# Optimization experiments

Hardware: AMD Instinct MI355X
Metric: run time of the kernel (lower is better)

The kernel has to match this reference:

```python
import jax, jax.numpy as jnp
import numpy as np

B, L, C = 4, 1024, 512
H, DK, DV, NF = 8, 64, 192, 192


def _sinusoid_basis(seq_len, nf):
    # distances -(L-1)..(L-1), sinusoidal feature basis of width nf
    d = jnp.arange(-(seq_len - 1), seq_len, dtype=jnp.float32)[:, None]  # [2L-1,1]
    half = nf // 2
    freqs = jnp.exp(-jnp.arange(half, dtype=jnp.float32) * (np.log(10000.0) / half))
    ang = d * freqs[None, :]
    return jnp.concatenate([jnp.sin(ang), jnp.cos(ang)], axis=-1)  # [2L-1, nf]


def setup_inputs() -> dict:
    key = jax.random.key(0)
    ks = jax.random.split(key, 12)
    s = lambda fan: 1.0 / np.sqrt(fan)
    return {
        "x": jax.random.normal(ks[0], (B, L, C), jnp.float32),
        "Wq": jax.random.normal(ks[1], (C, H * DK), jnp.float32) * s(C),
        "bq": jnp.zeros((H * DK,), jnp.float32),
        "Wk": jax.random.normal(ks[2], (C, H * DK), jnp.float32) * s(C),
        "bk": jnp.zeros((H * DK,), jnp.float32),
        "Wv": jax.random.normal(ks[3], (C, H * DV), jnp.float32) * s(C),
        "bv": jnp.zeros((H * DV,), jnp.float32),
        "Wo": jax.random.normal(ks[4], (H * DV, C), jnp.float32) * s(H * DV),
        "bo": jnp.zeros((C,), jnp.float32),
        "We": jax.random.normal(ks[5], (NF, DK), jnp.float32) * s(NF),
        "u": jax.random.normal(ks[6], (H, DK), jnp.float32) * 0.02,
        "v": jax.random.normal(ks[7], (H, DK), jnp.float32) * 0.02,
    }


def reference(x, Wq, bq, Wk, bk, Wv, bv, Wo, bo, We, u, v):
    b, l, c = x.shape
    Q = (x @ Wq + bq).reshape(b, l, H, DK).transpose(0, 2, 1, 3)  # [b,h,l,dk]
    K = (x @ Wk + bk).reshape(b, l, H, DK).transpose(0, 2, 1, 3)
    V = (x @ Wv + bv).reshape(b, l, H, DV).transpose(0, 2, 1, 3)  # [b,h,l,dv]

    R = _sinusoid_basis(l, NF) @ We  # [2l-1, dk], index r <-> distance r-(l-1)

    # rel-shift gather: shifted[i,j] = raw[i, j - i + (l-1)] (relative distance j-i)
    idx = (jnp.arange(l)[None, :] - jnp.arange(l)[:, None]) + (l - 1)  # [l,l]

    term1 = jnp.einsum('bhid,bhjd->bhij', Q, K)                 # content-content
    t2 = jnp.einsum('bhid,rd->bhir', Q, R)                      # [b,h,l,2l-1]
    term2 = jnp.take_along_axis(t2, jnp.broadcast_to(idx[None, None], (b, H, l, l)), axis=-1)
    term3 = jnp.einsum('hd,bhjd->bhj', u, K)[:, :, None, :]     # content bias [b,h,1,l]
    t4 = jnp.einsum('hd,rd->hr', v, R)                          # [h,2l-1]
    term4 = jnp.take(t4, idx, axis=1)[None]                     # [1,h,l,l]

    attn = jax.nn.softmax(term1 + term2 + term3 + term4, axis=-1)
    out = jnp.einsum('bhij,bhjd->bhid', attn, V)                # [b,h,l,dv]
    out = out.transpose(0, 2, 1, 3).reshape(b, l, H * DV)
    return out @ Wo + bo
```

## Files before the change

### kernel.cpp

```cpp
#include <hip/hip_runtime.h>
#include <cstdint>
#include <cstddef>

#define B_   4
#define L_   1024
#define H_   8
#define DK_  64
#define DV_  192
#define HALF_ 96
#define LOG2E_ 1.44269504088896f

typedef _Float16 half8 __attribute__((ext_vector_type(8)));
typedef _Float16 half4v __attribute__((ext_vector_type(4)));
typedef float f32x4 __attribute__((ext_vector_type(4)));

__device__ __forceinline__ void gll16(const void* g, void* lds) {
    __builtin_amdgcn_global_load_lds(
        (const __attribute__((address_space(1))) unsigned int*)g,
        (__attribute__((address_space(3))) unsigned int*)lds, 16, 0, 0);
}

__global__ void k_prologue(const float* __restrict__ x, _Float16* __restrict__ xh,
                           const float* __restrict__ We, _Float16* __restrict__ Weh,
                           const float* __restrict__ Wq, const float* __restrict__ Wk,
                           const float* __restrict__ Wv, const float* __restrict__ Wo,
                           _Float16* __restrict__ Wqkvt, _Float16* __restrict__ Wot,
                           const float* __restrict__ bq, const float* __restrict__ bk,
                           const float* __restrict__ bv, float* __restrict__ bqkv,
                           float* __restrict__ Tsin, float* __restrict__ Tcos,
                           const float* __restrict__ v, float* __restrict__ vWe) {
    __shared__ float tile[64][65];
    const int t = blockIdx.x, tid = threadIdx.x;
    if (t < 2048) {
        int i = t * 256 + tid;
        float4 vv = ((const float4*)x)[i];
        half4v h;
        h[0] = (_Float16)vv.x; h[1] = (_Float16)vv.y; h[2] = (_Float16)vv.z; h[3] = (_Float16)vv.w;
        ((half4v*)xh)[i] = h;
    } else if (t < 2060) {
        int i = (t - 2048) * 256 + tid;
        if (i < 192 * 64 / 4) {
            float4 vv = ((const float4*)We)[i];
            half4v h;
            h[0] = (_Float16)vv.x; h[1] = (_Float16)vv.y; h[2] = (_Float16)vv.z; h[3] = (_Float16)vv.w;
            ((half4v*)Weh)[i] = h;
        }
    } else if (t < 2572) {
        const float* src; _Float16* dst; int K, N, bx, by;
        if (t < 2124)      { int rel = t - 2060; src = Wq; dst = Wqkvt;                       K = 512;  N = 512;  bx = rel & 7;   by = rel >> 3; }
        else if (t < 2188) { int rel = t - 2124; src = Wk; dst = Wqkvt + (size_t)512 * 512;   K = 512;  N = 512;  bx = rel & 7;   by = rel >> 3; }
        else if (t < 2380) { int rel = t - 2188; src = Wv; dst = Wqkvt + (size_t)1024 * 512;  K = 512;  N = 1536; bx = rel % 24;  by = rel / 24; }
        else               { int rel = t - 2380; src = Wo; dst = Wot;                         K = 1536; N = 512;  bx = rel & 7;   by = rel >> 3; }
        int n0 = bx << 6, k0 = by << 6;
#pragma unroll
        for (int q = 0; q < 16; ++q) {
            int e = (q << 8) + tid;
            int r = e >> 6, c = e & 63;
            tile[r][c] = src[(size_t)(k0 + r) * N + n0 + c];
        }
        __syncthreads();
#pragma unroll
        for (int q = 0; q < 16; ++q) {
            int e = (q << 8) + tid;
            int r = e >> 6, c = e & 63;
            dst[(size_t)(n0 + r) * K + k0 + c] = (_Float16)tile[c][r];
        }
    } else if (t < 2582) {
        int i = (t - 2572) * 256 + tid;
        if (i < 2560) {
            float vv;
            if (i < 512) vv = bq[i];
            else if (i < 1024) vv = bk[i - 512];
            else vv = bv[i - 1024];
            bqkv[i] = vv;
        }
    } else if (t < 2966) {
        int idx = (t - 2582) * 256 + tid;
        if (idx < L_ * HALF_) {
            int i = idx / HALF_;
            int f = idx - i * HALF_;
            float w = expf(-(float)f * 0.09594104554141865f);
            float a = (float)i * w;
            Tsin[idx] = sinf(a);
            Tcos[idx] = cosf(a);
        }
    } else {
        int idx = (t - 2966) * 256 + tid;
        if (idx < 8 * 192) {
            int h = idx / 192, f = idx - h * 192;
            float acc = 0.f;
#pragma unroll
            for (int k4 = 0; k4 < 16; ++k4) {
                float4 vv = *(const float4*)(v + (h << 6) + (k4 << 2));
                float4 we = *(const float4*)(We + (size_t)f * 64 + (k4 << 2));
                acc += vv.x * we.x + vv.y * we.y + vv.z * we.z + vv.w * we.w;
            }
            vWe[idx] = acc;
        }
    }
}

template<int TNB, bool OUT_F16, bool GMODE>
__global__ __launch_bounds__(256) void k_gemm2(
    const _Float16* __restrict__ A, const _Float16* __restrict__ Bt,
    const float* __restrict__ bias, void* __restrict__ Cout,
    int M, int N, int K, int nbx)
{
    constexpr int BUFSZ = 16384 + TNB * 128;
    __shared__ char sm[2 * BUFSZ];
    const int nwg = gridDim.x;
    const int bid = blockIdx.x;
    const int sw = (bid & 7) * (nwg >> 3) + (bid >> 3);
    const int bx = sw % nbx, by = sw / nbx;
    const int m0 = by << 7, n0 = bx * TNB;
    const int tid = threadIdx.x;
    const int lane = tid & 63, l15 = lane & 15, g = lane >> 4;
    const int w = tid >> 6;
    constexpr int AM = (TNB == 128) ? 4 : 2;
    constexpr int BJ = (TNB >= 64) ? 4 : 2;
    const int wm = (TNB == 128) ? ((w >> 1) << 6) : (w << 5);
    const int wn = (TNB == 128) ? ((w & 1) << 6) : 0;

    f32x4 acc[AM][BJ] = {};

    auto stage = [&](int kt, int bufsel) {
        char* As = sm + bufsel * BUFSZ;
        char* Bs = As + 16384;
#pragma unroll
        for (int i2 = 0; i2 < 4; ++i2) {
            int byte = (i2 << 12) + (tid << 4);
            int row = byte >> 7, bso = byte & 127;
            size_t a_off;
            if constexpr (GMODE) {
                int rg = m0 + row;
                a_off = ((((size_t)(rg >> 13) << 10) + (rg & 1023)) * 2560 + (((rg >> 10) & 7) << 6) + (kt << 6)) * 2;
            } else {
                a_off = ((size_t)(m0 + row) * K + (kt << 6)) * 2;
            }
            gll16((const char*)A + a_off + (bso ^ ((row & 7) << 4)), As + byte);
        }
        const char* Bg = (const char*)Bt + ((size_t)n0 * K + (kt << 6)) * 2;
#pragma unroll
        for (int i2 = 0; i2 < (TNB >> 5); ++i2) {
            int byte = (i2 << 12) + (tid << 4);
            int row = byte >> 7, bso = byte & 127;
            gll16(Bg + (size_t)row * (K * 2) + (bso ^ ((row & 7) << 4)), Bs + byte);
        }
    };

    const int nk = K >> 6;
    stage(0, 0);
    __syncthreads();
    for (int kt = 0; kt < nk; ++kt) {
        const int cur = kt & 1;
        if (kt + 1 < nk) stage(kt + 1, cur ^ 1);
        const char* As = sm + cur * BUFSZ;
        const char* Bs = As + 16384;
#pragma unroll
        for (int kq = 0; kq < 2; ++kq) {
            half8 af[AM], bf[BJ];
#pragma unroll
            for (int a = 0; a < AM; ++a) {
                int row = wm + (a << 4) + l15;
                af[a] = *(const half8*)(As + (row << 7) + ((((kq << 2) | g) ^ (row & 7)) << 4));
            }
#pragma unroll
            for (int bj = 0; bj < BJ; ++bj) {
                int row = wn + (bj << 4) + l15;
                bf[bj] = *(const half8*)(Bs + (row << 7) + ((((kq << 2) | g) ^ (row & 7)) << 4));
            }
#pragma unroll
            for (int a = 0; a < AM; ++a)
#pragma unroll
                for (int bj = 0; bj < BJ; ++bj)
                    acc[a][bj] = __builtin_amdgcn_mfma_f32_16x16x32_f16(af[a], bf[bj], acc[a][bj], 0, 0, 0);
        }
        __syncthreads();
    }
#pragma unroll
    for (int a = 0; a < AM; ++a)
#pragma unroll
        for (int bj = 0; bj < BJ; ++bj)
#pragma unroll
            for (int r = 0; r < 4; ++r) {
                int row = m0 + wm + (a << 4) + (g << 2) + r;
                int col = n0 + wn + (bj << 4) + l15;
                float bb;
                if constexpr (GMODE) bb = bias[(((m0 >> 10) & 7) * N) + col];
                else                 bb = bias ? bias[col] : 0.0f;
                float vv = acc[a][bj][r] + bb;
                if (OUT_F16) ((_Float16*)Cout)[(size_t)row * N + col] = (_Float16)vv;
                else         ((float*)Cout)[(size_t)row * N + col] = vv;
            }
}

__global__ void k_build(const _Float16* __restrict__ QKVh, const _Float16* __restrict__ Gf,
                        const float* __restrict__ Tsin, const float* __restrict__ Tcos,
                        const float* __restrict__ u,
                        _Float16* __restrict__ Qext, _Float16* __restrict__ Kext,
                        float* __restrict__ bias3, _Float16* __restrict__ Vd) {
    __shared__ float tile[64][65];
    const int t = blockIdx.x, tid = threadIdx.x;
    if (t < 8192) {
        const bool isQ = (t < 4096);
        int r = ((isQ ? t : t - 4096) << 3) + (tid >> 5);
        int cc = tid & 31;
        int i = r & 1023, h = (r >> 10) & 7, b = r >> 13;
        half8 val;
        if (cc < 8) {
            if (isQ) {
                half8 q = *(const half8*)(QKVh + ((size_t)(b << 10) + i) * 2560 + (h << 6) + (cc << 3));
#pragma unroll
                for (int z = 0; z < 8; ++z) val[z] = (_Float16)((float)q[z] * LOG2E_);
            } else {
                val = *(const half8*)(QKVh + ((size_t)(b << 10) + i) * 2560 + 512 + (h << 6) + (cc << 3));
                float4 u0 = *(const float4*)(u + (h << 6) + (cc << 3));
                float4 u1 = *(const float4*)(u + (h << 6) + (cc << 3) + 4);
                float p = (float)val[0] * u0.x + (float)val[1] * u0.y + (float)val[2] * u0.z + (float)val[3] * u0.w
                        + (float)val[4] * u1.x + (float)val[5] * u1.y + (float)val[6] * u1.z + (float)val[7] * u1.w;
                p += __shfl_xor(p, 1); p += __shfl_xor(p, 2); p += __shfl_xor(p, 4);
                if (cc == 0) bias3[r] = p * LOG2E_;
            }
        } else {
            int f = (cc < 20) ? ((cc - 8) << 3) : ((cc - 20) << 3);
            if (isQ) {
                half8 g0 = *(const half8*)(Gf + (size_t)r * 192 + f);
                half8 g1 = *(const half8*)(Gf + (size_t)r * 192 + 96 + f);
                float4 s0 = *(const float4*)(Tsin + i * 96 + f);
                float4 s1 = *(const float4*)(Tsin + i * 96 + f + 4);
                float4 c0 = *(const float4*)(Tcos + i * 96 + f);
                float4 c1 = *(const float4*)(Tcos + i * 96 + f + 4);
                float sv[8] = {s0.x, s0.y, s0.z, s0.w, s1.x, s1.y, s1.z, s1.w};
                float cv[8] = {c0.x, c0.y, c0.z, c0.w, c1.x, c1.y, c1.z, c1.w};
                if (cc < 20) {
#pragma unroll
                    for (int z = 0; z < 8; ++z) val[z] = (_Float16)(((float)g0[z] * cv[z] + (float)g1[z] * sv[z]) * LOG2E_);
                } else {
#pragma unroll
                    for (int z = 0; z < 8; ++z) val[z] = (_Float16)(((float)g1[z] * cv[z] - (float)g0[z] * sv[z]) * LOG2E_);
                }
            } else {
                const float* T = (cc < 20) ? Tsin : Tcos;
                float4 t0 = *(const float4*)(T + i * 96 + f);
                float4 t1 = *(const float4*)(T + i * 96 + f + 4);
                float tv[8] = {t0.x, t0.y, t0.z, t0.w, t1.x, t1.y, t1.z, t1.w};
#pragma unroll
                for (int z = 0; z < 8; ++z) val[z] = (_Float16)tv[z];
            }
        }
        _Float16* dst = isQ ? Qext : Kext;
        *(half8*)((char*)dst + (size_t)r * 512 + ((cc ^ (r & 7)) << 4)) = val;
    } else {
        int rel = t - 8192;
        int jx = rel & 15, rest = rel >> 4;
        int dy = rest % 3, bh = rest / 3;
        int j0 = jx << 6, d0 = dy << 6;
        int b = bh >> 3, h = bh & 7;
#pragma unroll
        for (int q = 0; q < 16; ++q) {
            int e = (q << 8) + tid;
            int r = e >> 6, c = e & 63;
            tile[r][c] = (float)QKVh[((size_t)(b << 10) + j0 + r) * 2560 + 1024 + h * 192 + d0 + c];
        }
        __syncthreads();
        char* outb = (char*)Vd + (size_t)bh * 192 * 2048;
#pragma unroll
        for (int q = 0; q < 2; ++q) {
            int e = (q << 8) + tid;
            int dr = e >> 3, jc = e & 7;
            int d = d0 + dr;
            half8 v;
#pragma unroll
            for (int z = 0; z < 8; ++z) v[z] = (_Float16)tile[(jc << 3) + z][dr];
            *(half8*)(outb + (size_t)d * 2048 + (j0 << 1) + ((jc ^ (d & 7)) << 4)) = v;
        }
    }
}

__global__ __attribute__((amdgpu_flat_work_group_size(1024, 1024)))
void k_attn(
    const _Float16* __restrict__ Qext, const _Float16* __restrict__ Kext,
    const _Float16* __restrict__ Vd, const float* __restrict__ bias3,
    _Float16* __restrict__ AOh)
{
    __shared__ char smem[131072];

    const int bid = blockIdx.x;
    const int sw = ((bid & 7) << 5) + (bid >> 3);
    const int bh = sw >> 3;
    const int i0 = (sw & 7) << 7;
    const int tid = threadIdx.x;
    const int w = tid >> 6, lane = tid & 63, l15 = lane & 15, g = lane >> 4;
    const int rowg = w & 7, jhalf = w >> 3;
    const int b = bh >> 3, h = bh & 7;

    const char* Kg = (const char*)Kext + ((size_t)bh << 10) * 512;
    const char* Vg = (const char*)Vd + (size_t)bh * 192 * 2048;
    const float* b3g = bias3 + (bh << 10);
    char* Pw = smem + 114688 + (w << 10);

    half8 qf[8];
    {
        int row = i0 + (rowg << 4) + l15;
        const char* qp = (const char*)Qext + ((size_t)(bh << 10) + row) * 512;
#pragma unroll
        for (int kq = 0; kq < 8; ++kq)
            qf[kq] = *(const half8*)(qp + ((((kq << 2) + g) ^ (row & 7)) << 4));
    }

    f32x4 oacc[12] = {};
    float m_run[4], l_lane[4];
#pragma unroll
    for (int r = 0; r < 4; ++r) { m_run[r] = -3.0e38f; l_lane[r] = 0.f; }

    auto stage = [&](int jt, int bufsel) {
        char* Kb = smem + bufsel * 32768;
        char* Vb = smem + 65536 + bufsel * 24576;
        const char* Ksrc = Kg + (size_t)jt * 32768;
#pragma unroll
        for (int i2 = 0; i2 < 2; ++i2) {
            int byte = (i2 << 14) + (tid << 4);
            gll16(Ksrc + byte, Kb + byte);
        }
        {
            int byte = tid << 4;
            int d = byte >> 7, c = byte & 127;
            gll16(Vg + (size_t)d * 2048 + (jt << 7) + c, Vb + byte);
        }
        if (tid < 512) {
            int byte = 16384 + (tid << 4);
            int d = byte >> 7, c = byte & 127;
            gll16(Vg + (size_t)d * 2048 + (jt << 7) + c, Vb + byte);
        }
    };

    stage(0, 0);
    __syncthreads();

    for (int jt = 0; jt < 16; ++jt) {
        const int cur = jt & 1;
        if (jt + 1 < 16) stage(jt + 1, cur ^ 1);
        const char* Kb = smem + cur * 32768;
        const char* Vb = smem + 65536 + cur * 24576;

        f32x4 s[2];
#pragma unroll
        for (int jn = 0; jn < 2; ++jn) {
            float b3 = b3g[(jt << 6) + (jhalf << 5) + (jn << 4) + l15];
            s[jn] = (f32x4){b3, b3, b3, b3};
        }
        __builtin_amdgcn_s_setprio(1);
#pragma unroll
        for (int kq = 0; kq < 8; ++kq) {
#pragma unroll
            for (int jn = 0; jn < 2; ++jn) {
                int krow = (((jhalf << 1) + jn) << 4) + l15;
                half8 bf = *(const half8*)(Kb + (krow << 9) + ((((kq << 2) + g) ^ (krow & 7)) << 4));
                s[jn] = __builtin_amdgcn_mfma_f32_16x16x32_f16(qf[kq], bf, s[jn], 0, 0, 0);
            }
        }
        __builtin_amdgcn_s_setprio(0);
        bool pass = true;
#pragma unroll
        for (int jn = 0; jn < 2; ++jn)
#pragma unroll
            for (int r = 0; r < 4; ++r) pass &= (s[jn][r] <= m_run[r] + 8.0f);
        if (!__all(pass)) {
#pragma unroll
            for (int r = 0; r < 4; ++r) {
                float tm = fmaxf(s[0][r], s[1][r]);
                tm = fmaxf(tm, __shfl_xor(tm, 1));
                tm = fmaxf(tm, __shfl_xor(tm, 2));
                tm = fmaxf(tm, __shfl_xor(tm, 4));
                tm = fmaxf(tm, __shfl_xor(tm, 8));
                float mnew = fmaxf(m_run[r], tm);
                float al = exp2f(m_run[r] - mnew);
                l_lane[r] *= al;
                m_run[r] = mnew;
#pragma unroll
                for (int dn = 0; dn < 12; ++dn) oacc[dn][r] *= al;
            }
        }
#pragma unroll
        for (int jn = 0; jn < 2; ++jn)
#pragma unroll
            for (int r = 0; r < 4; ++r) {
                float p = exp2f(s[jn][r] - m_run[r]);
                l_lane[r] += p;
                int row = (g << 2) + r;
                int c = ((jn << 1) + (l15 >> 3)) ^ g;
                *(_Float16*)(Pw + (row << 6) + (c << 4) + ((l15 & 7) << 1)) = (_Float16)p;
            }
        half8 pa;
        {
            int c = g ^ ((l15 >> 2) & 3);
            pa = *(const half8*)(Pw + (l15 << 6) + (c << 4));
        }
        __builtin_amdgcn_s_setprio(1);
#pragma unroll
        for (int dn = 0; dn < 12; ++dn) {
            int d = (dn << 4) + l15;
            half8 vb = *(const half8*)(Vb + (d << 7) + ((((jhalf << 2) + g) ^ (d & 7)) << 4));
            oacc[dn] = __builtin_amdgcn_mfma_f32_16x16x32_f16(pa, vb, oacc[dn], 0, 0, 0);
        }
        __builtin_amdgcn_s_setprio(0);
        __syncthreads();
    }

    float l_run[4];
#pragma unroll
    for (int r = 0; r < 4; ++r) {
        float l = l_lane[r];
        l += __shfl_xor(l, 1);
        l += __shfl_xor(l, 2);
        l += __shfl_xor(l, 4);
        l += __shfl_xor(l, 8);
        l_run[r] = l;
    }

    float* Cml = (float*)smem;
    float* Co  = (float*)(smem + 2048);
#pragma unroll
    for (int r = 0; r < 4; ++r)
        if (l15 == 0) {
            int rowi = (rowg << 4) + (g << 2) + r;
            Cml[(((jhalf << 7) + rowi) << 1) + 0] = m_run[r];
            Cml[(((jhalf << 7) + rowi) << 1) + 1] = l_run[r];
        }
    __syncthreads();
    float fs[4], lt[4];
#pragma unroll
    for (int r = 0; r < 4; ++r) {
        int rowi = (rowg << 4) + (g << 2) + r;
        float mo = Cml[((((1 - jhalf) << 7) + rowi) << 1) + 0];
        float lo = Cml[((((1 - jhalf) << 7) + rowi) << 1) + 1];
        float M = fmaxf(m_run[r], mo);
        float f0 = exp2f(m_run[r] - M);
        float f1 = exp2f(mo - M);
        fs[r] = f0;
        lt[r] = l_run[r] * f0 + lo * f1;
    }
    if (jhalf == 1) {
#pragma unroll
        for (int dn = 0; dn < 12; ++dn)
#pragma unroll
            for (int r = 0; r < 4; ++r) {
                int rowi = (rowg << 4) + (g << 2) + r;
                Co[rowi * 196 + (dn << 4) + l15] = oacc[dn][r] * fs[r];
            }
    }
    __syncthreads();
    if (jhalf == 0) {
#pragma unroll
        for (int r = 0; r < 4; ++r) {
            int rowi = (rowg << 4) + (g << 2) + r;
            float inv = 1.0f / lt[r];
#pragma unroll
            for (int dn = 0; dn < 12; ++dn) {
                float ov = (oacc[dn][r] * fs[r] + Co[rowi * 196 + (dn << 4) + l15]) * inv;
                AOh[((size_t)(b << 10) + i0 + rowi) * 1536 + h * 192 + (dn << 4) + l15] = (_Float16)ov;
            }
        }
    }
}

extern "C" void kernel_launch(void* const* d_in, const int* in_sizes, int n_in,
                              void* d_out, int out_size, void* d_ws, size_t ws_size,
                              hipStream_t stream) {
    const float* x  = (const float*)d_in[0];
    const float* Wq = (const float*)d_in[1];
    const float* bq = (const float*)d_in[2];
    const float* Wk = (const float*)d_in[3];
    const float* bk = (const float*)d_in[4];
    const float* Wv = (const float*)d_in[5];
    const float* bv = (const float*)d_in[6];
    const float* Wo = (const float*)d_in[7];
    const float* bo = (const float*)d_in[8];
    const float* We = (const float*)d_in[9];
    const float* u  = (const float*)d_in[10];
    const float* v  = (const float*)d_in[11];
    float* out = (float*)d_out;

    char* ws = (char*)d_ws;
    size_t off = 0;
    auto alloc = [&](size_t bytes) -> void* {
        void* p = ws + off;
        off += (bytes + 255) & ~(size_t)255;
        return p;
    };
    _Float16* xh    = (_Float16*)alloc((size_t)4096 * 512 * 2);
    _Float16* Weh   = (_Float16*)alloc((size_t)192 * 64 * 2);
    _Float16* Wqkvt = (_Float16*)alloc((size_t)2560 * 512 * 2);
    _Float16* Wot   = (_Float16*)alloc((size_t)512 * 1536 * 2);
    float*    bqkv  = (float*)alloc((size_t)2560 * 4);
    float*    Tsin  = (float*)alloc((size_t)1024 * 96 * 4);
    float*    Tcos  = (float*)alloc((size_t)1024 * 96 * 4);
    float*    vWe   = (float*)alloc((size_t)8 * 192 * 4);
    _Float16* QKVh  = (_Float16*)alloc((size_t)4096 * 2560 * 2);
    _Float16* Gf16  = (_Float16*)alloc((size_t)32768 * 192 * 2);
    _Float16* Qext  = (_Float16*)alloc((size_t)32768 * 256 * 2);
    _Float16* Kext  = (_Float16*)alloc((size_t)32768 * 256 * 2);
    float*    bias3 = (float*)alloc((size_t)32768 * 4);
    _Float16* Vd    = (_Float16*)alloc((size_t)32 * 192 * 1024 * 2);
    _Float16* AOh   = (_Float16*)alloc((size_t)4096 * 1536 * 2);
    if (off > ws_size) return;

    k_prologue<<<2972, 256, 0, stream>>>(x, xh, We, Weh, Wq, Wk, Wv, Wo,
                                         Wqkvt, Wot, bq, bk, bv, bqkv, Tsin, Tcos, v, vWe);

    k_gemm2<128, true, false><<<640, 256, 0, stream>>>(xh, Wqkvt, bqkv, QKVh, 4096, 2560, 512, 20);

    k_gemm2<64, true, true><<<768, 256, 0, stream>>>(QKVh, Weh, vWe, Gf16, 32768, 192, 64, 3);

    k_build<<<9728, 256, 0, stream>>>(QKVh, Gf16, Tsin, Tcos, u, Qext, Kext, bias3, Vd);

    k_attn<<<256, 1024, 0, stream>>>(Qext, Kext, Vd, bias3, AOh);

    k_gemm2<32, false, false><<<512, 256, 0, stream>>>(AOh, Wot, bo, out, 4096, 512, 1536, 16);
}
```

Measured before the change: 147.4 us.

## Share one trig table across heads instead of replicating extended K

```diff
diff --git a/kernel.cpp b/kernel.cpp
--- a/kernel.cpp
+++ b/kernel.cpp
@@ -28,7 +28,8 @@
                            const float* __restrict__ bq, const float* __restrict__ bk,
                            const float* __restrict__ bv, float* __restrict__ bqkv,
                            float* __restrict__ Tsin, float* __restrict__ Tcos,
-                           const float* __restrict__ v, float* __restrict__ vWe) {
+                           const float* __restrict__ v, float* __restrict__ vWe,
+                           _Float16* __restrict__ Ctrig) {
     __shared__ float tile[64][65];
     const int t = blockIdx.x, tid = threadIdx.x;
     if (t < 2048) {
@@ -84,7 +85,7 @@
             Tsin[idx] = sinf(a);
             Tcos[idx] = cosf(a);
         }
-    } else {
+    } else if (t < 2972) {
         int idx = (t - 2966) * 256 + tid;
         if (idx < 8 * 192) {
             int h = idx / 192, f = idx - h * 192;
@@ -96,6 +97,21 @@
                 acc += vv.x * we.x + vv.y * we.y + vv.z * we.z + vv.w * we.w;
             }
             vWe[idx] = acc;
+        }
+    } else {
+        int idx = (t - 2972) * 256 + tid;
+        if (idx < 1024 * 24) {
+            int j = idx / 24, lc = idx - j * 24;
+            int f0 = (lc < 12) ? (lc << 3) : ((lc - 12) << 3);
+            half8 val;
+#pragma unroll
+            for (int z = 0; z < 8; ++z) {
+                float w = expf(-(float)(f0 + z) * 0.09594104554141865f);
+                float a = (float)j * w;
+                val[z] = (_Float16)((lc < 12) ? sinf(a) : cosf(a));
+            }
+            int pos = ((lc >> 3) << 3) + ((lc & 7) ^ (j & 7));
+            *(half8*)((char*)Ctrig + (size_t)j * 384 + (pos << 4)) = val;
         }
     }
 }
@@ -197,61 +213,52 @@
 __global__ void k_build(const _Float16* __restrict__ QKVh, const _Float16* __restrict__ Gf,
                         const float* __restrict__ Tsin, const float* __restrict__ Tcos,
                         const float* __restrict__ u,
-                        _Float16* __restrict__ Qext, _Float16* __restrict__ Kext,
+                        _Float16* __restrict__ Qext, _Float16* __restrict__ Ksmall,
                         float* __restrict__ bias3, _Float16* __restrict__ Vd) {
     __shared__ float tile[64][65];
     const int t = blockIdx.x, tid = threadIdx.x;
-    if (t < 8192) {
-        const bool isQ = (t < 4096);
-        int r = ((isQ ? t : t - 4096) << 3) + (tid >> 5);
+    if (t < 4096) {
+        int r = (t << 3) + (tid >> 5);
         int cc = tid & 31;
         int i = r & 1023, h = (r >> 10) & 7, b = r >> 13;
         half8 val;
         if (cc < 8) {
-            if (isQ) {
-                half8 q = *(const half8*)(QKVh + ((size_t)(b << 10) + i) * 2560 + (h << 6) + (cc << 3));
-#pragma unroll
-                for (int z = 0; z < 8; ++z) val[z] = (_Float16)((float)q[z] * LOG2E_);
-            } else {
-                val = *(const half8*)(QKVh + ((size_t)(b << 10) + i) * 2560 + 512 + (h << 6) + (cc << 3));
-                float4 u0 = *(const float4*)(u + (h << 6) + (cc << 3));
-                float4 u1 = *(const float4*)(u + (h << 6) + (cc << 3) + 4);
-                float p = (float)val[0] * u0.x + (float)val[1] * u0.y + (float)val[2] * u0.z + (float)val[3] * u0.w
-                        + (float)val[4] * u1.x + (float)val[5] * u1.y + (float)val[6] * u1.z + (float)val[7] * u1.w;
-                p += __shfl_xor(p, 1); p += __shfl_xor(p, 2); p += __shfl_xor(p, 4);
-                if (cc == 0) bias3[r] = p * LOG2E_;
-            }
+            half8 q = *(const half8*)(QKVh + ((size_t)(b << 10) + i) * 2560 + (h << 6) + (cc << 3));
+#pragma unroll
+            for (int z = 0; z < 8; ++z) val[z] = (_Float16)((float)q[z] * LOG2E_);
         } else {
             int f = (cc < 20) ? ((cc - 8) << 3) : ((cc - 20) << 3);
-            if (isQ) {
-                half8 g0 = *(const half8*)(Gf + (size_t)r * 192 + f);
-                half8 g1 = *(const half8*)(Gf + (size_t)r * 192 + 96 + f);
-                float4 s0 = *(const float4*)(Tsin + i * 96 + f);
-                float4 s1 = *(const float4*)(Tsin + i * 96 + f + 4);
-                float4 c0 = *(const float4*)(Tcos + i * 96 + f);
-                float4 c1 = *(const float4*)(Tcos + i * 96 + f + 4);
-                float sv[8] = {s0.x, s0.y, s0.z, s0.w, s1.x, s1.y, s1.z, s1.w};
-                float cv[8] = {c0.x, c0.y, c0.z, c0.w, c1.x, c1.y, c1.z, c1.w};
-                if (cc < 20) {
-#pragma unroll
-                    for (int z = 0; z < 8; ++z) val[z] = (_Float16)(((float)g0[z] * cv[z] + (float)g1[z] * sv[z]) * LOG2E_);
-                } else {
-#pragma unroll
-                    for (int z = 0; z < 8; ++z) val[z] = (_Float16)(((float)g1[z] * cv[z] - (float)g0[z] * sv[z]) * LOG2E_);
-                }
+            half8 g0 = *(const half8*)(Gf + (size_t)r * 192 + f);
+            half8 g1 = *(const half8*)(Gf + (size_t)r * 192 + 96 + f);
+            float4 s0 = *(const float4*)(Tsin + i * 96 + f);
+            float4 s1 = *(const float4*)(Tsin + i * 96 + f + 4);
+            float4 c0 = *(const float4*)(Tcos + i * 96 + f);
+            float4 c1 = *(const float4*)(Tcos + i * 96 + f + 4);
+            float sv[8] = {s0.x, s0.y, s0.z, s0.w, s1.x, s1.y, s1.z, s1.w};
+            float cv[8] = {c0.x, c0.y, c0.z, c0.w, c1.x, c1.y, c1.z, c1.w};
+            if (cc < 20) {
+#pragma unroll
+                for (int z = 0; z < 8; ++z) val[z] = (_Float16)(((float)g0[z] * cv[z] + (float)g1[z] * sv[z]) * LOG2E_);
             } else {
-                const float* T = (cc < 20) ? Tsin : Tcos;
-                float4 t0 = *(const float4*)(T + i * 96 + f);
-                float4 t1 = *(const float4*)(T + i * 96 + f + 4);
-                float tv[8] = {t0.x, t0.y, t0.z, t0.w, t1.x, t1.y, t1.z, t1.w};
-#pragma unroll
-                for (int z = 0; z < 8; ++z) val[z] = (_Float16)tv[z];
-            }
-        }
-        _Float16* dst = isQ ? Qext : Kext;
-        *(half8*)((char*)dst + (size_t)r * 512 + ((cc ^ (r & 7)) << 4)) = val;
+#pragma unroll
+                for (int z = 0; z < 8; ++z) val[z] = (_Float16)(((float)g1[z] * cv[z] - (float)g0[z] * sv[z]) * LOG2E_);
+            }
+        }
+        *(half8*)((char*)Qext + (size_t)r * 512 + ((cc ^ (r & 7)) << 4)) = val;
+    } else if (t < 5120) {
+        int r = ((t - 4096) << 5) + (tid >> 3);
+        int cc = tid & 7;
+        int i = r & 1023, h = (r >> 10) & 7, b = r >> 13;
+        half8 val = *(const half8*)(QKVh + ((size_t)(b << 10) + i) * 2560 + 512 + (h << 6) + (cc << 3));
+        float4 u0 = *(const float4*)(u + (h << 6) + (cc << 3));
+        float4 u1 = *(const float4*)(u + (h << 6) + (cc << 3) + 4);
+        float p = (float)val[0] * u0.x + (float)val[1] * u0.y + (float)val[2] * u0.z + (float)val[3] * u0.w
+                + (float)val[4] * u1.x + (float)val[5] * u1.y + (float)val[6] * u1.z + (float)val[7] * u1.w;
+        p += __shfl_xor(p, 1); p += __shfl_xor(p, 2); p += __shfl_xor(p, 4);
+        if (cc == 0) bias3[r] = p * LOG2E_;
+        *(half8*)((char*)Ksmall + (size_t)r * 128 + ((cc ^ (r & 7)) << 4)) = val;
     } else {
-        int rel = t - 8192;
+        int rel = t - 5120;
         int jx = rel & 15, rest = rel >> 4;
         int dy = rest % 3, bh = rest / 3;
         int j0 = jx << 6, d0 = dy << 6;
@@ -279,7 +286,8 @@
 
 __global__ __attribute__((amdgpu_flat_work_group_size(1024, 1024)))
 void k_attn(
-    const _Float16* __restrict__ Qext, const _Float16* __restrict__ Kext,
+    const _Float16* __restrict__ Qext, const _Float16* __restrict__ Ksmall,
+    const _Float16* __restrict__ Ctrig,
     const _Float16* __restrict__ Vd, const float* __restrict__ bias3,
     _Float16* __restrict__ AOh)
 {
@@ -294,7 +302,8 @@
     const int rowg = w & 7, jhalf = w >> 3;
     const int b = bh >> 3, h = bh & 7;
 
-    const char* Kg = (const char*)Kext + ((size_t)bh << 10) * 512;
+    const char* Ksm = (const char*)Ksmall + ((size_t)bh << 10) * 128;
+    const char* Ctg = (const char*)Ctrig;
     const char* Vg = (const char*)Vd + (size_t)bh * 192 * 2048;
     const float* b3g = bias3 + (bh << 10);
     char* Pw = smem + 114688 + (w << 10);
@@ -316,11 +325,15 @@
     auto stage = [&](int jt, int bufsel) {
         char* Kb = smem + bufsel * 32768;
         char* Vb = smem + 65536 + bufsel * 24576;
-        const char* Ksrc = Kg + (size_t)jt * 32768;
+        const int cc = tid & 31;
 #pragma unroll
         for (int i2 = 0; i2 < 2; ++i2) {
             int byte = (i2 << 14) + (tid << 4);
-            gll16(Ksrc + byte, Kb + byte);
+            int j = (jt << 6) + (byte >> 9);
+            const char* src = (cc < 8)
+                ? Ksm + (size_t)j * 128 + (cc << 4)
+                : Ctg + (size_t)j * 384 + ((cc - 8) << 4);
+            gll16(src, Kb + byte);
         }
         {
             int byte = tid << 4;
@@ -488,33 +501,34 @@
         off += (bytes + 255) & ~(size_t)255;
         return p;
     };
-    _Float16* xh    = (_Float16*)alloc((size_t)4096 * 512 * 2);
-    _Float16* Weh   = (_Float16*)alloc((size_t)192 * 64 * 2);
-    _Float16* Wqkvt = (_Float16*)alloc((size_t)2560 * 512 * 2);
-    _Float16* Wot   = (_Float16*)alloc((size_t)512 * 1536 * 2);
-    float*    bqkv  = (float*)alloc((size_t)2560 * 4);
-    float*    Tsin  = (float*)alloc((size_t)1024 * 96 * 4);
-    float*    Tcos  = (float*)alloc((size_t)1024 * 96 * 4);
-    float*    vWe   = (float*)alloc((size_t)8 * 192 * 4);
-    _Float16* QKVh  = (_Float16*)alloc((size_t)4096 * 2560 * 2);
-    _Float16* Gf16  = (_Float16*)alloc((size_t)32768 * 192 * 2);
-    _Float16* Qext  = (_Float16*)alloc((size_t)32768 * 256 * 2);
-    _Float16* Kext  = (_Float16*)alloc((size_t)32768 * 256 * 2);
-    float*    bias3 = (float*)alloc((size_t)32768 * 4);
-    _Float16* Vd    = (_Float16*)alloc((size_t)32 * 192 * 1024 * 2);
-    _Float16* AOh   = (_Float16*)alloc((size_t)4096 * 1536 * 2);
+    _Float16* xh     = (_Float16*)alloc((size_t)4096 * 512 * 2);
+    _Float16* Weh    = (_Float16*)alloc((size_t)192 * 64 * 2);
+    _Float16* Wqkvt  = (_Float16*)alloc((size_t)2560 * 512 * 2);
+    _Float16* Wot    = (_Float16*)alloc((size_t)512 * 1536 * 2);
+    float*    bqkv   = (float*)alloc((size_t)2560 * 4);
+    float*    Tsin   = (float*)alloc((size_t)1024 * 96 * 4);
+    float*    Tcos   = (float*)alloc((size_t)1024 * 96 * 4);
+    float*    vWe    = (float*)alloc((size_t)8 * 192 * 4);
+    _Float16* Ctrig  = (_Float16*)alloc((size_t)1024 * 192 * 2);
+    _Float16* QKVh   = (_Float16*)alloc((size_t)4096 * 2560 * 2);
+    _Float16* Gf16   = (_Float16*)alloc((size_t)32768 * 192 * 2);
+    _Float16* Qext   = (_Float16*)alloc((size_t)32768 * 256 * 2);
+    _Float16* Ksmall = (_Float16*)alloc((size_t)32768 * 64 * 2);
+    float*    bias3  = (float*)alloc((size_t)32768 * 4);
+    _Float16* Vd     = (_Float16*)alloc((size_t)32 * 192 * 1024 * 2);
+    _Float16* AOh    = (_Float16*)alloc((size_t)4096 * 1536 * 2);
     if (off > ws_size) return;
 
-    k_prologue<<<2972, 256, 0, stream>>>(x, xh, We, Weh, Wq, Wk, Wv, Wo,
-                                         Wqkvt, Wot, bq, bk, bv, bqkv, Tsin, Tcos, v, vWe);
+    k_prologue<<<3068, 256, 0, stream>>>(x, xh, We, Weh, Wq, Wk, Wv, Wo,
+                                         Wqkvt, Wot, bq, bk, bv, bqkv, Tsin, Tcos, v, vWe, Ctrig);
 
     k_gemm2<128, true, false><<<640, 256, 0, stream>>>(xh, Wqkvt, bqkv, QKVh, 4096, 2560, 512, 20);
 
     k_gemm2<64, true, true><<<768, 256, 0, stream>>>(QKVh, Weh, vWe, Gf16, 32768, 192, 64, 3);
 
-    k_build<<<9728, 256, 0, stream>>>(QKVh, Gf16, Tsin, Tcos, u, Qext, Kext, bias3, Vd);
-
-    k_attn<<<256, 1024, 0, stream>>>(Qext, Kext, Vd, bias3, AOh);
+    k_build<<<6656, 256, 0, stream>>>(QKVh, Gf16, Tsin, Tcos, u, Qext, Ksmall, bias3, Vd);
+
+    k_attn<<<256, 1024, 0, stream>>>(Qext, Ksmall, Ctrig, Vd, bias3, AOh);
 
     k_gemm2<32, false, false><<<512, 256, 0, stream>>>(AOh, Wot, bo, out, 4096, 512, 1536, 16);
 }
```

Result: slower. 163.3 us (+10.8%).
